# Kernel optimization log

Hardware: AMD Instinct MI355X
Metric: run time of the kernel (lower is better)

The kernel has to match this reference:

```python
import jax, jax.numpy as jnp
import numpy as np

STATE_LEN = 4096
SEQ_LEN = 8192
T = 1024  # number of time buckets in time_sim_mat


def setup_inputs() -> dict:
    key = jax.random.key(0)
    k1, k2, k3 = jax.random.split(key, 3)
    his = jax.random.randint(k1, (SEQ_LEN,), 0, T, dtype=jnp.int64 if jax.config.jax_enable_x64 else jnp.int32)
    cur = jax.random.randint(k2, (STATE_LEN,), 0, T, dtype=jnp.int64 if jax.config.jax_enable_x64 else jnp.int32)
    time_sim_mat = jax.random.normal(k3, (T, T), dtype=jnp.float32)
    return {"his": his, "cur": cur, "time_sim_mat": time_sim_mat}


def reference(his, cur, time_sim_mat):
    # attn_energies[i, j] = time_sim_mat[cur[i], his[j]]  (vectorized gather)
    energies = time_sim_mat[cur[:, None], his[None, :]]  # [state_len, seq_len]
    return jax.nn.softmax(energies, axis=-1)
```

## Files before the change

kernel.cpp:

```cpp
#include <hip/hip_runtime.h>
#include <cstddef>

#define TDIM 1024
#define SEQ 8192
#define NROWS 4096

typedef float f32x4 __attribute__((ext_vector_type(4)));

__global__ __launch_bounds__(256) void fused_kernel(
    const int* __restrict__ his, const int* __restrict__ cur,
    const float* __restrict__ M, float* __restrict__ out)
{
    __shared__ int lc[TDIM];
    __shared__ float red[8];
    float* prob = (float*)lc;

    const int tid = threadIdx.x;
    const int row = blockIdx.x;
    const int r = cur[row];
    const float* Mrow = M + (size_t)r * TDIM;

#pragma unroll
    for (int k = 0; k < 4; ++k) lc[tid + 256 * k] = 0;

    const int4* his4 = (const int4*)his;
    int4 h[8];
#pragma unroll
    for (int it = 0; it < 8; ++it) h[it] = his4[it * 256 + tid];

    float m[4];
#pragma unroll
    for (int k = 0; k < 4; ++k) m[k] = Mrow[tid + 256 * k];

    __syncthreads();

#pragma unroll
    for (int it = 0; it < 8; ++it) {
        atomicAdd(&lc[h[it].x], 1);
        atomicAdd(&lc[h[it].y], 1);
        atomicAdd(&lc[h[it].z], 1);
        atomicAdd(&lc[h[it].w], 1);
    }
    __syncthreads();

    int c[4];
#pragma unroll
    for (int k = 0; k < 4; ++k) c[k] = lc[tid + 256 * k];

    float lmax = -3.402823466e38f;
#pragma unroll
    for (int k = 0; k < 4; ++k)
        if (c[k] > 0) lmax = fmaxf(lmax, m[k]);
#pragma unroll
    for (int off = 32; off > 0; off >>= 1)
        lmax = fmaxf(lmax, __shfl_down(lmax, off, 64));
    const int wave = tid >> 6, lane = tid & 63;
    if (lane == 0) red[wave] = lmax;
    __syncthreads();
    const float gmax = fmaxf(fmaxf(red[0], red[1]), fmaxf(red[2], red[3]));

    float e[4];
    float lsum = 0.f;
#pragma unroll
    for (int k = 0; k < 4; ++k) {
        e[k] = __expf(m[k] - gmax);
        lsum += (float)c[k] * e[k];
    }
#pragma unroll
    for (int off = 32; off > 0; off >>= 1)
        lsum += __shfl_down(lsum, off, 64);
    if (lane == 0) red[4 + wave] = lsum;
    __syncthreads();
    const float inv = 1.0f / (red[4] + red[5] + red[6] + red[7]);

#pragma unroll
    for (int k = 0; k < 4; ++k)
        prob[tid + 256 * k] = e[k] * inv;
    __syncthreads();

    f32x4* out4 = (f32x4*)(out + (size_t)row * SEQ);
#pragma unroll
    for (int it = 0; it < 8; ++it) {
        f32x4 o;
        o.x = prob[h[it].x];
        o.y = prob[h[it].y];
        o.z = prob[h[it].z];
        o.w = prob[h[it].w];
        out4[it * 256 + tid] = o;
    }
}

extern "C" void kernel_launch(void* const* d_in, const int* in_sizes, int n_in,
                              void* d_out, int out_size, void* d_ws, size_t ws_size,
                              hipStream_t stream) {
    const int*   his = (const int*)d_in[0];
    const int*   cur = (const int*)d_in[1];
    const float* M   = (const float*)d_in[2];
    float* out = (float*)d_out;
    (void)d_ws; (void)ws_size;

    fused_kernel<<<NROWS, 256, 0, stream>>>(his, cur, M, out);
}
```

Measured before the change: 143.6 us.

## Compute softmax once per distinct cur value and broadcast to matching rows

Launches one block per time bucket instead of per output row. Each block scans cur to collect the rows that map to its bucket, computes the histogram-weighted softmax once, and writes the same result to every matching output row. This removes redundant histogram, reduction and exp work for duplicate cur values. In exchange, every block reads all of cur, and the number of writes per block varies with duplicate counts, which can unbalance load.

```diff
diff --git a/kernel.cpp b/kernel.cpp
--- a/kernel.cpp
+++ b/kernel.cpp
@@ -7,32 +7,46 @@
 
 typedef float f32x4 __attribute__((ext_vector_type(4)));
 
-__global__ __launch_bounds__(256) void fused_kernel(
+__global__ __launch_bounds__(256) void unique_fused_kernel(
     const int* __restrict__ his, const int* __restrict__ cur,
     const float* __restrict__ M, float* __restrict__ out)
 {
     __shared__ int lc[TDIM];
     __shared__ float red[8];
+    __shared__ int mrows[NROWS];
+    __shared__ int mcount;
     float* prob = (float*)lc;
 
     const int tid = threadIdx.x;
-    const int row = blockIdx.x;
-    const int r = cur[row];
-    const float* Mrow = M + (size_t)r * TDIM;
+    const int r = blockIdx.x;
+
+    if (tid == 0) mcount = 0;
+#pragma unroll
+    for (int k = 0; k < 4; ++k) lc[tid + 256 * k] = 0;
+    __syncthreads();
 
 #pragma unroll
-    for (int k = 0; k < 4; ++k) lc[tid + 256 * k] = 0;
+    for (int k = 0; k < 16; ++k) {
+        int row = tid + 256 * k;
+        if (cur[row] == r) {
+            int idx = atomicAdd(&mcount, 1);
+            mrows[idx] = row;
+        }
+    }
 
     const int4* his4 = (const int4*)his;
     int4 h[8];
 #pragma unroll
     for (int it = 0; it < 8; ++it) h[it] = his4[it * 256 + tid];
 
+    const float* Mrow = M + (size_t)r * TDIM;
     float m[4];
 #pragma unroll
     for (int k = 0; k < 4; ++k) m[k] = Mrow[tid + 256 * k];
 
     __syncthreads();
+    const int nm = mcount;
+    if (nm == 0) return;
 
 #pragma unroll
     for (int it = 0; it < 8; ++it) {
@@ -78,15 +92,21 @@
         prob[tid + 256 * k] = e[k] * inv;
     __syncthreads();
 
-    f32x4* out4 = (f32x4*)(out + (size_t)row * SEQ);
+    f32x4 o[8];
 #pragma unroll
     for (int it = 0; it < 8; ++it) {
-        f32x4 o;
-        o.x = prob[h[it].x];
-        o.y = prob[h[it].y];
-        o.z = prob[h[it].z];
-        o.w = prob[h[it].w];
-        out4[it * 256 + tid] = o;
+        o[it].x = prob[h[it].x];
+        o[it].y = prob[h[it].y];
+        o[it].z = prob[h[it].z];
+        o[it].w = prob[h[it].w];
+    }
+
+    for (int mi = 0; mi < nm; ++mi) {
+        int row = mrows[mi];
+        f32x4* out4 = (f32x4*)(out + (size_t)row * SEQ);
+#pragma unroll
+        for (int it = 0; it < 8; ++it)
+            out4[it * 256 + tid] = o[it];
     }
 }
 
@@ -99,5 +119,5 @@
     float* out = (float*)d_out;
     (void)d_ws; (void)ws_size;
 
-    fused_kernel<<<NROWS, 256, 0, stream>>>(his, cur, M, out);
+    unique_fused_kernel<<<TDIM, 256, 0, stream>>>(his, cur, M, out);
 }
```

After: 147.2 us. 1.02x slower.

## Replace histogram-based softmax with online softmax over gathered row values

Applied to the files above, without the earlier changes.

Drops the per-block LDS histogram built with atomics and the two-pass max/sum over bins. Each thread now gathers its 32 values from the cached M row in LDS, computes a local max and exp-sum, and merges them across lanes and waves with an online-softmax reduction. The final probabilities are scaled from registers instead of re-gathered from LDS. This removes 8192 LDS atomics per block and a barrier, at the cost of 32 exps per thread instead of 4 and higher register pressure.

```diff
diff --git a/kernel.cpp b/kernel.cpp
--- a/kernel.cpp
+++ b/kernel.cpp
@@ -11,81 +11,76 @@
     const int* __restrict__ his, const int* __restrict__ cur,
     const float* __restrict__ M, float* __restrict__ out)
 {
-    __shared__ int lc[TDIM];
-    __shared__ float red[8];
-    float* prob = (float*)lc;
+    __shared__ float mrow[TDIM];
+    __shared__ float redm[4];
+    __shared__ float reds[4];
 
     const int tid = threadIdx.x;
     const int row = blockIdx.x;
     const int r = cur[row];
     const float* Mrow = M + (size_t)r * TDIM;
 
-#pragma unroll
-    for (int k = 0; k < 4; ++k) lc[tid + 256 * k] = 0;
-
     const int4* his4 = (const int4*)his;
     int4 h[8];
 #pragma unroll
     for (int it = 0; it < 8; ++it) h[it] = his4[it * 256 + tid];
 
-    float m[4];
 #pragma unroll
-    for (int k = 0; k < 4; ++k) m[k] = Mrow[tid + 256 * k];
-
+    for (int k = 0; k < 4; ++k) mrow[tid + 256 * k] = Mrow[tid + 256 * k];
     __syncthreads();
 
+    float g[32];
 #pragma unroll
     for (int it = 0; it < 8; ++it) {
-        atomicAdd(&lc[h[it].x], 1);
-        atomicAdd(&lc[h[it].y], 1);
-        atomicAdd(&lc[h[it].z], 1);
-        atomicAdd(&lc[h[it].w], 1);
+        g[4 * it + 0] = mrow[h[it].x];
+        g[4 * it + 1] = mrow[h[it].y];
+        g[4 * it + 2] = mrow[h[it].z];
+        g[4 * it + 3] = mrow[h[it].w];
     }
+
+    float mloc = g[0];
+#pragma unroll
+    for (int j = 1; j < 32; ++j) mloc = fmaxf(mloc, g[j]);
+    float e[32];
+    float s = 0.f;
+#pragma unroll
+    for (int j = 0; j < 32; ++j) {
+        e[j] = __expf(g[j] - mloc);
+        s += e[j];
+    }
+
+    float m = mloc;
+#pragma unroll
+    for (int off = 32; off > 0; off >>= 1) {
+        float om = __shfl_xor(m, off, 64);
+        float os = __shfl_xor(s, off, 64);
+        float nm_ = fmaxf(m, om);
+        s = s * __expf(m - nm_) + os * __expf(om - nm_);
+        m = nm_;
+    }
+
+    const int wave = tid >> 6, lane = tid & 63;
+    if (lane == 0) { redm[wave] = m; reds[wave] = s; }
     __syncthreads();
+    float M0 = redm[0], S0 = reds[0];
+#pragma unroll
+    for (int w = 1; w < 4; ++w) {
+        float mw = redm[w], sw = reds[w];
+        float nm_ = fmaxf(M0, mw);
+        S0 = S0 * __expf(M0 - nm_) + sw * __expf(mw - nm_);
+        M0 = nm_;
+    }
 
-    int c[4];
-#pragma unroll
-    for (int k = 0; k < 4; ++k) c[k] = lc[tid + 256 * k];
-
-    float lmax = -3.402823466e38f;
-#pragma unroll
-    for (int k = 0; k < 4; ++k)
-        if (c[k] > 0) lmax = fmaxf(lmax, m[k]);
-#pragma unroll
-    for (int off = 32; off > 0; off >>= 1)
-        lmax = fmaxf(lmax, __shfl_down(lmax, off, 64));
-    const int wave = tid >> 6, lane = tid & 63;
-    if (lane == 0) red[wave] = lmax;
-    __syncthreads();
-    const float gmax = fmaxf(fmaxf(red[0], red[1]), fmaxf(red[2], red[3]));
-
-    float e[4];
-    float lsum = 0.f;
-#pragma unroll
-    for (int k = 0; k < 4; ++k) {
-        e[k] = __expf(m[k] - gmax);
-        lsum += (float)c[k] * e[k];
-    }
-#pragma unroll
-    for (int off = 32; off > 0; off >>= 1)
-        lsum += __shfl_down(lsum, off, 64);
-    if (lane == 0) red[4 + wave] = lsum;
-    __syncthreads();
-    const float inv = 1.0f / (red[4] + red[5] + red[6] + red[7]);
-
-#pragma unroll
-    for (int k = 0; k < 4; ++k)
-        prob[tid + 256 * k] = e[k] * inv;
-    __syncthreads();
+    const float scale = __expf(mloc - M0) / S0;
 
     f32x4* out4 = (f32x4*)(out + (size_t)row * SEQ);
 #pragma unroll
     for (int it = 0; it < 8; ++it) {
         f32x4 o;
-        o.x = prob[h[it].x];
-        o.y = prob[h[it].y];
-        o.z = prob[h[it].z];
-        o.w = prob[h[it].w];
+        o.x = e[4 * it + 0] * scale;
+        o.y = e[4 * it + 1] * scale;
+        o.z = e[4 * it + 2] * scale;
+        o.w = e[4 * it + 3] * scale;
         out4[it * 256 + tid] = o;
     }
 }
```

Measured after the change: 143.9 us (median of 2 runs). About the same (+0.2%).
